# Performance work log

Hardware: AMD Instinct MI355X
Metric: run time of the kernel (lower is better)

Reference implementation:

```python
import jax, jax.numpy as jnp
import numpy as np

NEG_SLOPE = 0.2
# relation r: src node type SRC[r], dst node type DST[r]; 0=Drug, 1=Disease
# order: TREATS, TREATED_BY, HAS_CONTRAIND, CONTRAIND_BY, HAS_PARENTCODE, HAS_CHILDCODE, INTERACTS
SRC = (0, 1, 0, 1, 1, 1, 0)
DST = (1, 0, 1, 0, 1, 1, 0)

N_DRUG, N_DIS, D_IN, HID, OUT, E = 20000, 40000, 256, 128, 128, 150000


def _gat(x_src, x_dst, edge_index, Ws, Wd, a_s, a_d, b):
    # single-head PyG GATConv, add_self_loops=False
    hs = x_src @ Ws                      # [Ns, H]
    hd = x_dst @ Wd                      # [Nd, H]
    src, dst = edge_index[0], edge_index[1]
    n_dst = x_dst.shape[0]
    alpha_src = hs @ a_s                 # [Ns]
    alpha_dst = hd @ a_d                 # [Nd]
    alpha = jax.nn.leaky_relu(alpha_src[src] + alpha_dst[dst], NEG_SLOPE)  # [E]
    amax = jax.ops.segment_max(alpha, dst, num_segments=n_dst)
    amax = jnp.where(jnp.isfinite(amax), amax, 0.0)
    ex = jnp.exp(alpha - amax[dst])
    denom = jax.ops.segment_sum(ex, dst, num_segments=n_dst)
    coef = ex / (denom[dst] + 1e-16)     # per-destination softmax (PyG softmax)
    out = jax.ops.segment_sum(hs[src] * coef[:, None], dst, num_segments=n_dst)
    return out + b


def _hetero_layer(xd, xi, edges, Ws, Wd, a_s, a_d, b):
    feats = (xd, xi)
    H = b.shape[1]
    outs = [jnp.zeros((xd.shape[0], H), xd.dtype), jnp.zeros((xi.shape[0], H), xi.dtype)]
    for r in range(7):
        o = _gat(feats[SRC[r]], feats[DST[r]], edges[r], Ws[r], Wd[r], a_s[r], a_d[r], b[r])
        outs[DST[r]] = outs[DST[r]] + o   # HeteroConv aggr='sum'
    return outs[0], outs[1]


def setup_inputs() -> dict:
    key = jax.random.key(0)
    ks = jax.random.split(key, 32)
    x_drug = jax.random.normal(ks[0], (N_DRUG, D_IN), jnp.float32)
    x_disease = jax.random.normal(ks[1], (N_DIS, D_IN), jnp.float32)
    nsz = (N_DRUG, N_DIS)
    edges = []
    for r in range(7):
        s = jax.random.randint(ks[2 + 2 * r], (E,), 0, nsz[SRC[r]], jnp.int32)
        d = jax.random.randint(ks[3 + 2 * r], (E,), 0, nsz[DST[r]], jnp.int32)
        edges.append(jnp.stack([s, d]))
    s = 0.1
    W1s = s * jax.random.normal(ks[16], (7, D_IN, HID), jnp.float32)
    W1d = s * jax.random.normal(ks[17], (7, D_IN, HID), jnp.float32)
    W1d = W1d.at[6].set(W1s[6])  # INTERACTS shares src/dst lin (GATConv(-1,...))
    a1s = s * jax.random.normal(ks[18], (7, HID), jnp.float32)
    a1d = s * jax.random.normal(ks[19], (7, HID), jnp.float32)
    b1 = jnp.zeros((7, HID), jnp.float32)
    W2s = s * jax.random.normal(ks[20], (7, HID, HID), jnp.float32)
    W2d = s * jax.random.normal(ks[21], (7, HID, HID), jnp.float32)
    W2d = W2d.at[6].set(W2s[6])
    a2s = s * jax.random.normal(ks[22], (7, HID), jnp.float32)
    a2d = s * jax.random.normal(ks[23], (7, HID), jnp.float32)
    b2 = jnp.zeros((7, HID), jnp.float32)
    W_drug = s * jax.random.normal(ks[24], (HID, OUT), jnp.float32)
    b_drug = jnp.zeros((OUT,), jnp.float32)
    W_dis = s * jax.random.normal(ks[25], (HID, OUT), jnp.float32)
    b_dis = jnp.zeros((OUT,), jnp.float32)
    return {"x_drug": x_drug, "x_disease": x_disease,
            "e_treats": edges[0], "e_treated_by": edges[1], "e_contraind": edges[2],
            "e_contraind_by": edges[3], "e_parent": edges[4], "e_child": edges[5],
            "e_interacts": edges[6],
            "W1s": W1s, "W1d": W1d, "a1s": a1s, "a1d": a1d, "b1": b1,
            "W2s": W2s, "W2d": W2d, "a2s": a2s, "a2d": a2d, "b2": b2,
            "W_drug": W_drug, "b_drug": b_drug, "W_dis": W_dis, "b_dis": b_dis}


def reference(x_drug, x_disease, e_treats, e_treated_by, e_contraind, e_contraind_by,
              e_parent, e_child, e_interacts,
              W1s, W1d, a1s, a1d, b1, W2s, W2d, a2s, a2d, b2,
              W_drug, b_drug, W_dis, b_dis):
    edges = (e_treats, e_treated_by, e_contraind, e_contraind_by, e_parent, e_child, e_interacts)
    xd, xi = _hetero_layer(x_drug, x_disease, edges, W1s, W1d, a1s, a1d, b1)
    xd, xi = jax.nn.relu(xd), jax.nn.relu(xi)  # dropout is identity (eval mode)
    xd, xi = _hetero_layer(xd, xi, edges, W2s, W2d, a2s, a2d, b2)
    out_drug = jax.nn.relu(xd @ W_drug + b_drug)
    out_disease = jax.nn.relu(xi @ W_dis + b_dis)
    return out_drug, out_disease
```

## Files before the change

kernel.cpp:

```cpp
#include <hip/hip_runtime.h>
#include <stdint.h>

#define NDRUG 20000
#define NDIS  40000
#define HID   128
#define NE    150000
#define NREL  7
#define RPSTR (NDIS + 1)
#define NS_TOT (NREL * RPSTR)

typedef unsigned short ushort_t;
typedef __attribute__((ext_vector_type(8))) short bf16x8;
typedef __attribute__((ext_vector_type(4))) float f32x4;
typedef const __attribute__((address_space(1))) void gv_t;
typedef __attribute__((address_space(3))) void lv_t;

__device__ __forceinline__ ushort_t f2bf(float f) {
  unsigned u = __float_as_uint(f);
  u += 0x7FFFu + ((u >> 16) & 1u);
  return (ushort_t)(u >> 16);
}
__device__ __forceinline__ float bf2f(ushort_t h) {
  return __uint_as_float(((unsigned)h) << 16);
}

struct GemmJob { const ushort_t* A; const ushort_t* BT; const float* bias; void* C; int M, N; };

template<bool BIAS, bool RELU, bool BF16OUT>
__global__ __launch_bounds__(256) void gemm_dual(GemmJob j0, GemmJob j1, int gx0, int K)
{
  __shared__ ushort_t As[128 * 32];
  __shared__ ushort_t Bs[128 * 32];
  const bool first = blockIdx.x < (unsigned)gx0;
  const GemmJob J = first ? j0 : j1;
  const int bx = first ? blockIdx.x : blockIdx.x - gx0;
  if ((int)blockIdx.y * 128 >= J.N) return;
  const int tid = threadIdx.x;
  const int m0 = bx * 128;
  const int n0 = blockIdx.y * 128;
  const int wave = tid >> 6, lane = tid & 63;
  const int wm = wave & 1, wn = wave >> 1;
  const int l15 = lane & 15, lk = lane >> 4;

  const int rowS = wave * 16 + (lane >> 2);
  const int chunk = (lane & 3) * 8;
  const int grA0 = min(m0 + rowS, J.M - 1);
  const int grA1 = min(m0 + rowS + 64, J.M - 1);
  const ushort_t* ga0 = J.A + (size_t)grA0 * K + chunk;
  const ushort_t* ga1 = J.A + (size_t)grA1 * K + chunk;
  const ushort_t* gb0 = J.BT + (size_t)(n0 + rowS) * K + chunk;
  const ushort_t* gb1 = J.BT + (size_t)(n0 + rowS + 64) * K + chunk;

  f32x4 acc[4][4] = {};

  for (int k0 = 0; k0 < K; k0 += 32) {
    __syncthreads();
    __builtin_amdgcn_global_load_lds((gv_t*)(ga0 + k0), (lv_t*)(As + wave * 512), 16, 0, 0);
    __builtin_amdgcn_global_load_lds((gv_t*)(ga1 + k0), (lv_t*)(As + wave * 512 + 2048), 16, 0, 0);
    __builtin_amdgcn_global_load_lds((gv_t*)(gb0 + k0), (lv_t*)(Bs + wave * 512), 16, 0, 0);
    __builtin_amdgcn_global_load_lds((gv_t*)(gb1 + k0), (lv_t*)(Bs + wave * 512 + 2048), 16, 0, 0);
    __syncthreads();

    bf16x8 af[4], bfg[4];
    #pragma unroll
    for (int m = 0; m < 4; ++m)
      af[m] = *reinterpret_cast<const bf16x8*>(&As[(wm * 64 + m * 16 + l15) * 32 + lk * 8]);
    #pragma unroll
    for (int n = 0; n < 4; ++n)
      bfg[n] = *reinterpret_cast<const bf16x8*>(&Bs[(wn * 64 + n * 16 + l15) * 32 + lk * 8]);
    #pragma unroll
    for (int m = 0; m < 4; ++m)
      #pragma unroll
      for (int n = 0; n < 4; ++n)
        acc[m][n] = __builtin_amdgcn_mfma_f32_16x16x32_bf16(af[m], bfg[n], acc[m][n], 0, 0, 0);
  }

  #pragma unroll
  for (int m = 0; m < 4; ++m) {
    int rbase = m0 + wm * 64 + m * 16 + lk * 4;
    #pragma unroll
    for (int n = 0; n < 4; ++n) {
      int col = n0 + wn * 64 + n * 16 + l15;
      float bv = 0.f;
      if (BIAS) bv = J.bias[col];
      #pragma unroll
      for (int j = 0; j < 4; ++j) {
        int row = rbase + j;
        if (row >= J.M) continue;
        float v = acc[m][n][j] + bv;
        if (RELU) v = fmaxf(v, 0.f);
        if (BF16OUT) ((ushort_t*)J.C)[(size_t)row * J.N + col] = f2bf(v);
        else         ((float*)J.C)[(size_t)row * J.N + col] = v;
      }
    }
  }
}

__global__ void build_wcat2(const float* __restrict__ WA, ushort_t* __restrict__ outA,
                            int ncolA, int4 relsA,
                            const float* __restrict__ WB, ushort_t* __restrict__ outB,
                            int ncolB, int4 relsB, int K)
{
  int id = blockIdx.x * 256 + threadIdx.x;
  const float* W; ushort_t* out; int ncol; int4 rels;
  int totA = K * ncolA;
  if (id < totA) { W = WA; out = outA; ncol = ncolA; rels = relsA; }
  else {
    id -= totA;
    if (id >= K * ncolB) return;
    W = WB; out = outB; ncol = ncolB; rels = relsB;
  }
  int k = id / ncol, c = id - k * ncol;
  int rr = (&rels.x)[c >> 7];
  out[(size_t)c * K + k] = f2bf(W[((size_t)rr * K + k) * HID + (c & 127)]);
}

__global__ __launch_bounds__(256) void wvec_kernel(
    const float* __restrict__ Wsrc, const float* __restrict__ as_,
    const float* __restrict__ Wdst, const float* __restrict__ ad_,
    float* __restrict__ wv, int K)
{
  int slot = blockIdx.x;
  int r = slot % NREL;
  const float* W = (slot < NREL ? Wsrc : Wdst) + (size_t)r * K * HID;
  const float* a = (slot < NREL ? as_ : ad_) + r * HID;
  int wave = threadIdx.x >> 6, lane = threadIdx.x & 63;
  int k = blockIdx.y * 4 + wave;
  if (k >= K) return;
  float s = W[(size_t)k * HID + lane] * a[lane]
          + W[(size_t)k * HID + 64 + lane] * a[64 + lane];
  #pragma unroll
  for (int off = 32; off; off >>= 1) s += __shfl_xor(s, off);
  if (lane == 0) wv[slot * 256 + k] = s;
}

__global__ void cvt2_f32_bf16(const float* __restrict__ inA, ushort_t* __restrict__ outA, int n8A,
                              const float* __restrict__ inB, ushort_t* __restrict__ outB, int n8B)
{
  int i = blockIdx.x * 256 + threadIdx.x;
  const float* in; ushort_t* out;
  if (i < n8A) { in = inA; out = outA; }
  else {
    i -= n8A;
    if (i >= n8B) return;
    in = inB; out = outB;
  }
  float4 a = reinterpret_cast<const float4*>(in)[2 * i];
  float4 b = reinterpret_cast<const float4*>(in)[2 * i + 1];
  ushort_t r[8] = {f2bf(a.x), f2bf(a.y), f2bf(a.z), f2bf(a.w),
                   f2bf(b.x), f2bf(b.y), f2bf(b.z), f2bf(b.w)};
  reinterpret_cast<uint4*>(out)[i] = *reinterpret_cast<uint4*>(r);
}

struct AlphaJobs { int wslot[8]; int outOff[8]; };

template<int K>
__global__ __launch_bounds__(256) void alpha_dual(
    const ushort_t* __restrict__ XD, const ushort_t* __restrict__ XI,
    const float* __restrict__ wv, float* __restrict__ outBase,
    AlphaJobs jd, AlphaJobs ji, int gbD)
{
  const bool isD = blockIdx.x < (unsigned)gbD;
  const ushort_t* X = isD ? XD : XI;
  const int N = isD ? NDRUG : NDIS;
  const AlphaJobs jobs = isD ? jd : ji;
  int i = (isD ? blockIdx.x : blockIdx.x - gbD) * 256 + threadIdx.x;
  if (i >= N) return;
  float acc[8];
  #pragma unroll
  for (int v = 0; v < 8; ++v) acc[v] = 0.f;
  const ushort_t* xp = X + (size_t)i * K;
  for (int k = 0; k < K; k += 8) {
    uint4 u = *reinterpret_cast<const uint4*>(xp + k);
    unsigned uu[4] = {u.x, u.y, u.z, u.w};
    float xf[8];
    #pragma unroll
    for (int q = 0; q < 4; ++q) {
      xf[2 * q]     = __uint_as_float(uu[q] << 16);
      xf[2 * q + 1] = __uint_as_float(uu[q] & 0xFFFF0000u);
    }
    #pragma unroll
    for (int v = 0; v < 8; ++v) {
      const float* wp = wv + jobs.wslot[v] * 256 + k;
      #pragma unroll
      for (int q = 0; q < 8; ++q) acc[v] += xf[q] * wp[q];
    }
  }
  #pragma unroll
  for (int v = 0; v < 8; ++v) outBase[jobs.outOff[v] + i] = acc[v];
}

struct RelIdx { const int* src[NREL]; const int* dst[NREL]; };
struct NdArr  { int nd[NREL]; };

__global__ void zero_ints(int* __restrict__ p, int n) {
  int i = blockIdx.x * 256 + threadIdx.x;
  if (i < n) p[i] = 0;
}
__global__ void hist_k(RelIdx ri, int* __restrict__ counts) {
  int e = blockIdx.x * 256 + threadIdx.x;
  int r = blockIdx.y;
  if (e >= NE) return;
  atomicAdd(&counts[r * RPSTR + ri.dst[r][e]], 1);
}
__global__ __launch_bounds__(256) void scan_blk(const int* __restrict__ in,
                                                int* __restrict__ partial,
                                                int* __restrict__ bsum, int n)
{
  __shared__ int ts[256];
  int t = threadIdx.x;
  int base = blockIdx.x * 1024 + t * 4;
  int v[4];
  #pragma unroll
  for (int i = 0; i < 4; ++i) v[i] = (base + i < n) ? in[base + i] : 0;
  int s = v[0] + v[1] + v[2] + v[3];
  ts[t] = s; __syncthreads();
  for (int off = 1; off < 256; off <<= 1) {
    int x = (t >= off) ? ts[t - off] : 0;
    __syncthreads();
    ts[t] += x;
    __syncthreads();
  }
  int run = ts[t] - s;
  #pragma unroll
  for (int i = 0; i < 4; ++i) {
    if (base + i < n) partial[base + i] = run;
    run += v[i];
  }
  if (t == 255) bsum[blockIdx.x] = ts[255];
}
__global__ __launch_bounds__(512) void scan_top(int* __restrict__ bsum, int nb) {
  __shared__ int ts[512];
  int t = threadIdx.x;
  int v = (t < nb) ? bsum[t] : 0;
  ts[t] = v; __syncthreads();
  for (int off = 1; off < 512; off <<= 1) {
    int x = (t >= off) ? ts[t - off] : 0;
    __syncthreads();
    ts[t] += x;
    __syncthreads();
  }
  if (t < nb) bsum[t] = ts[t] - v;
}
__global__ void scan_add(const int* __restrict__ partial, const int* __restrict__ bsum,
                         int* __restrict__ rowptr, int* __restrict__ cursor, int n)
{
  int i = blockIdx.x * 256 + threadIdx.x;
  if (i >= n) return;
  int v = partial[i] + bsum[i >> 10];
  rowptr[i] = v; cursor[i] = v;
}
__global__ void fill_k(RelIdx ri, int* __restrict__ cursor, int* __restrict__ colsrc) {
  int e = blockIdx.x * 256 + threadIdx.x;
  int r = blockIdx.y;
  if (e >= NE) return;
  int d = ri.dst[r][e];
  int pos = atomicAdd(&cursor[r * RPSTR + d], 1);
  colsrc[pos] = ri.src[r][e];
}

__global__ __launch_bounds__(256) void coef_k(
    const int* __restrict__ rowptr, const int* __restrict__ colsrc,
    float2* __restrict__ pack, const float* __restrict__ alphaB,
    float* __restrict__ invden, NdArr nds)
{
  int d = blockIdx.x * 256 + threadIdx.x;
  int r = blockIdx.y;
  if (d >= nds.nd[r]) return;
  int beg = rowptr[r * RPSTR + d], end = rowptr[r * RPSTR + d + 1];
  if (beg == end) return;
  const float ad = alphaB[(NREL + r) * NDIS + d];
  const float* as = alphaB + (size_t)r * NDIS;
  int deg = end - beg;
  float sum = 0.f;
  if (deg <= 16) {
    float av[16]; int sv[16];
    float m = -1e30f;
    #pragma unroll
    for (int i = 0; i < 16; ++i) {
      float a = -1e30f; int s = 0;
      if (i < deg) {
        s = colsrc[beg + i];
        a = as[s] + ad;
        a = a > 0.f ? a : 0.2f * a;
      }
      av[i] = a; sv[i] = s;
      m = fmaxf(m, a);
    }
    #pragma unroll
    for (int i = 0; i < 16; ++i) {
      if (i < deg) {
        float ex = __expf(av[i] - m);
        float2 pk; pk.x = ex; pk.y = __int_as_float(sv[i]);
        pack[beg + i] = pk;
        sum += ex;
      }
    }
  } else {
    float m = -1e30f;
    for (int i = beg; i < end; ++i) {
      float a = as[colsrc[i]] + ad;
      a = a > 0.f ? a : 0.2f * a;
      m = fmaxf(m, a);
    }
    for (int i = beg; i < end; ++i) {
      int s = colsrc[i];
      float a = as[s] + ad;
      a = a > 0.f ? a : 0.2f * a;
      float ex = __expf(a - m);
      float2 pk; pk.x = ex; pk.y = __int_as_float(s);
      pack[i] = pk;
      sum += ex;
    }
  }
  invden[r * NDIS + d] = 1.f / (sum + 1e-16f);
}

struct PvRel { int rel; int rowptr_off; const ushort_t* hs; int hst; int hoff; };
struct PvParams { PvRel dr[3]; PvRel di[4]; };

template<bool RELU>
__global__ __launch_bounds__(256) void pv_multi(
    PvParams P, const int* __restrict__ rowptr, const float2* __restrict__ pack,
    const float* __restrict__ invden, const float* __restrict__ bias,
    ushort_t* __restrict__ outD, ushort_t* __restrict__ outI, int nbD)
{
  const int wave = threadIdx.x >> 6, lane = threadIdx.x & 63;
  const int grp = lane >> 4, l15 = lane & 15;
  const int c0 = l15 * 8;
  const bool isD = blockIdx.x < (unsigned)nbD;
  const int d = (isD ? blockIdx.x : blockIdx.x - nbD) * 4 + wave;
  const int Nd = isD ? NDRUG : NDIS;
  if (d >= Nd) return;
  const int nr = isD ? 3 : 4;
  float acc[8] = {};

  #pragma unroll
  for (int q = 0; q < 4; ++q) {
    if (q >= nr) break;
    const PvRel R = isD ? P.dr[q] : P.di[q];
    const int beg = rowptr[R.rowptr_off + d];
    const int end = rowptr[R.rowptr_off + d + 1];
    if (beg == end) continue;
    const ushort_t* hsb = R.hs + R.hoff + c0;
    const int hst = R.hst;
    float p[8] = {};
    for (int c = beg; c < end; c += 8) {
      const int e0 = c + grp, e1 = c + 4 + grp;
      const float2 k0 = pack[min(e0, end - 1)];
      const float2 k1 = pack[min(e1, end - 1)];
      const float cf0 = (e0 < end) ? k0.x : 0.f;
      const float cf1 = (e1 < end) ? k1.x : 0.f;
      const uint4 h0 = *reinterpret_cast<const uint4*>(
          hsb + (size_t)__float_as_int(k0.y) * hst);
      const uint4 h1 = *reinterpret_cast<const uint4*>(
          hsb + (size_t)__float_as_int(k1.y) * hst);
      const unsigned w0[4] = {h0.x, h0.y, h0.z, h0.w};
      const unsigned w1[4] = {h1.x, h1.y, h1.z, h1.w};
      #pragma unroll
      for (int t = 0; t < 4; ++t) {
        p[2 * t]     += cf0 * __uint_as_float(w0[t] << 16);
        p[2 * t + 1] += cf0 * __uint_as_float(w0[t] & 0xFFFF0000u);
        p[2 * t]     += cf1 * __uint_as_float(w1[t] << 16);
        p[2 * t + 1] += cf1 * __uint_as_float(w1[t] & 0xFFFF0000u);
      }
    }
    const float inv = invden[R.rel * NDIS + d];
    #pragma unroll
    for (int t = 0; t < 8; ++t) acc[t] += p[t] * inv;
  }

  #pragma unroll
  for (int t = 0; t < 8; ++t) {
    acc[t] += __shfl_xor(acc[t], 16);
    acc[t] += __shfl_xor(acc[t], 32);
  }

  if (grp == 0) {
    #pragma unroll
    for (int q = 0; q < 4; ++q) {
      if (q >= nr) break;
      const PvRel R = isD ? P.dr[q] : P.di[q];
      const float4 b0 = *reinterpret_cast<const float4*>(&bias[R.rel * HID + c0]);
      const float4 b1 = *reinterpret_cast<const float4*>(&bias[R.rel * HID + c0 + 4]);
      acc[0] += b0.x; acc[1] += b0.y; acc[2] += b0.z; acc[3] += b0.w;
      acc[4] += b1.x; acc[5] += b1.y; acc[6] += b1.z; acc[7] += b1.w;
    }
    if (RELU) {
      #pragma unroll
      for (int t = 0; t < 8; ++t) acc[t] = fmaxf(acc[t], 0.f);
    }
    ushort_t o[8];
    #pragma unroll
    for (int t = 0; t < 8; ++t) o[t] = f2bf(acc[t]);
    ushort_t* out = isD ? outD : outI;
    *reinterpret_cast<uint4*>(out + (size_t)d * HID + c0) = *reinterpret_cast<uint4*>(o);
  }
}

static const int DSTh[NREL] = {1, 0, 1, 0, 1, 1, 0};

struct WsPlan {
  ushort_t *xdb1, *xib1, *xd1b, *xi1b, *xd2b, *xi2b;
  ushort_t *hs_d, *hs_i, *wcatT_d, *wcatT_i, *wfinT_d, *wfinT_i;
  float2* pack;
  float *alphaB, *wv, *invden;
  int *counts, *rowptr, *cursor, *colsrc, *bsum;
  size_t total_bytes;
};

static WsPlan plan_ws(void* d_ws) {
  WsPlan p;
  ushort_t* s = (ushort_t*)d_ws;
  p.xdb1 = s;     s += (size_t)NDRUG * 256;
  p.xib1 = s;     s += (size_t)NDIS * 256;
  p.xd1b = s;     s += (size_t)NDRUG * HID;
  p.xi1b = s;     s += (size_t)NDIS * HID;
  p.hs_d = s;     s += (size_t)NDRUG * 384;
  p.hs_i = s;     s += (size_t)NDIS * 512;
  p.wcatT_d = s;  s += 384 * 256;
  p.wcatT_i = s;  s += 512 * 256;
  p.wfinT_d = s;  s += 128 * 128;
  p.wfinT_i = s;  s += 128 * 128;
  p.xd2b = p.xdb1;
  p.xi2b = p.xib1;
  p.pack = (float2*)s;
  float2* e = p.pack + (size_t)NREL * NE;
  float* f = (float*)e;
  p.alphaB = f;   f += (size_t)15 * NDIS;
  p.wv = f;       f += 14 * 256;
  p.invden = f;   f += (size_t)NREL * NDIS;
  int* q = (int*)f;
  p.counts = q;   q += NS_TOT;
  p.rowptr = q;   q += NS_TOT;
  p.cursor = q;   q += NS_TOT;
  p.colsrc = q;   q += NREL * NE;
  p.bsum = q;     q += 512;
  p.total_bytes = (size_t)((char*)q - (char*)d_ws);
  return p;
}

static void run_layer(const ushort_t* XDb, const ushort_t* XIb, int K,
                      const float* Wsrc, const float* Wdst,
                      const float* as_, const float* ad_, const float* bias,
                      ushort_t* outDb, ushort_t* outIb, bool relu,
                      const WsPlan& p, hipStream_t stream)
{
  int4 rd = make_int4(0, 2, 6, 0);
  int4 ri4 = make_int4(1, 3, 4, 5);
  build_wcat2<<<(K * 896 + 255) / 256, 256, 0, stream>>>(
      Wsrc, p.wcatT_d, 384, rd, Wsrc, p.wcatT_i, 512, ri4, K);
  wvec_kernel<<<dim3(14, K / 4), 256, 0, stream>>>(Wsrc, as_, Wdst, ad_, p.wv, K);

  AlphaJobs jd = {};
  jd.wslot[0] = 0;     jd.outOff[0] = 0 * NDIS;
  jd.wslot[1] = 2;     jd.outOff[1] = 2 * NDIS;
  jd.wslot[2] = 6;     jd.outOff[2] = 6 * NDIS;
  jd.wslot[3] = 7 + 1; jd.outOff[3] = (7 + 1) * NDIS;
  jd.wslot[4] = 7 + 3; jd.outOff[4] = (7 + 3) * NDIS;
  jd.wslot[5] = 7 + 6; jd.outOff[5] = (7 + 6) * NDIS;
  jd.wslot[6] = 0;     jd.outOff[6] = 14 * NDIS;
  jd.wslot[7] = 0;     jd.outOff[7] = 14 * NDIS;
  AlphaJobs ji = {};
  ji.wslot[0] = 1;     ji.outOff[0] = 1 * NDIS;
  ji.wslot[1] = 3;     ji.outOff[1] = 3 * NDIS;
  ji.wslot[2] = 4;     ji.outOff[2] = 4 * NDIS;
  ji.wslot[3] = 5;     ji.outOff[3] = 5 * NDIS;
  ji.wslot[4] = 7 + 0; ji.outOff[4] = (7 + 0) * NDIS;
  ji.wslot[5] = 7 + 2; ji.outOff[5] = (7 + 2) * NDIS;
  ji.wslot[6] = 7 + 4; ji.outOff[6] = (7 + 4) * NDIS;
  ji.wslot[7] = 7 + 5; ji.outOff[7] = (7 + 5) * NDIS;
  int gbD = (NDRUG + 255) / 256, gbI = (NDIS + 255) / 256;
  if (K == 256)
    alpha_dual<256><<<gbD + gbI, 256, 0, stream>>>(XDb, XIb, p.wv, p.alphaB, jd, ji, gbD);
  else
    alpha_dual<128><<<gbD + gbI, 256, 0, stream>>>(XDb, XIb, p.wv, p.alphaB, jd, ji, gbD);

  GemmJob g0 = {XDb, p.wcatT_d, nullptr, p.hs_d, NDRUG, 384};
  GemmJob g1 = {XIb, p.wcatT_i, nullptr, p.hs_i, NDIS, 512};
  int gx0 = (NDRUG + 127) / 128, gx1 = (NDIS + 127) / 128;
  gemm_dual<false, false, true><<<dim3(gx0 + gx1, 4), 256, 0, stream>>>(g0, g1, gx0, K);

  NdArr nds;
  for (int r = 0; r < NREL; ++r) nds.nd[r] = DSTh[r] == 0 ? NDRUG : NDIS;
  coef_k<<<dim3((NDIS + 255) / 256, NREL), 256, 0, stream>>>(
      p.rowptr, p.colsrc, p.pack, p.alphaB, p.invden, nds);

  PvParams P;
  P.dr[0] = {1, 1 * RPSTR, p.hs_i, 512, 0};
  P.dr[1] = {3, 3 * RPSTR, p.hs_i, 512, 128};
  P.dr[2] = {6, 6 * RPSTR, p.hs_d, 384, 256};
  P.di[0] = {0, 0 * RPSTR, p.hs_d, 384, 0};
  P.di[1] = {2, 2 * RPSTR, p.hs_d, 384, 128};
  P.di[2] = {4, 4 * RPSTR, p.hs_i, 512, 256};
  P.di[3] = {5, 5 * RPSTR, p.hs_i, 512, 384};
  int nbD = (NDRUG + 3) / 4, nbI = (NDIS + 3) / 4;
  if (relu)
    pv_multi<true><<<nbD + nbI, 256, 0, stream>>>(
        P, p.rowptr, p.pack, p.invden, bias, outDb, outIb, nbD);
  else
    pv_multi<false><<<nbD + nbI, 256, 0, stream>>>(
        P, p.rowptr, p.pack, p.invden, bias, outDb, outIb, nbD);
}

extern "C" void kernel_launch(void* const* d_in, const int* in_sizes, int n_in,
                              void* d_out, int out_size, void* d_ws, size_t ws_size,
                              hipStream_t stream) {
  const float* x_drug = (const float*)d_in[0];
  const float* x_dis  = (const float*)d_in[1];
  RelIdx ri;
  for (int r = 0; r < NREL; ++r) {
    const int* e = (const int*)d_in[2 + r];
    ri.src[r] = e; ri.dst[r] = e + NE;
  }
  const float* W1s = (const float*)d_in[9];
  const float* W1d = (const float*)d_in[10];
  const float* a1s = (const float*)d_in[11];
  const float* a1d = (const float*)d_in[12];
  const float* b1  = (const float*)d_in[13];
  const float* W2s = (const float*)d_in[14];
  const float* W2d = (const float*)d_in[15];
  const float* a2s = (const float*)d_in[16];
  const float* a2d = (const float*)d_in[17];
  const float* b2  = (const float*)d_in[18];
  const float* Wdr = (const float*)d_in[19];
  const float* bdr = (const float*)d_in[20];
  const float* Wdi = (const float*)d_in[21];
  const float* bdi = (const float*)d_in[22];

  WsPlan p = plan_ws(d_ws);
  if (p.total_bytes > ws_size) return;

  cvt2_f32_bf16<<<((NDRUG + NDIS) * 256 / 8 + 255) / 256, 256, 0, stream>>>(
      x_drug, p.xdb1, NDRUG * 256 / 8, x_dis, p.xib1, NDIS * 256 / 8);

  zero_ints<<<(NS_TOT + 255) / 256, 256, 0, stream>>>(p.counts, NS_TOT);
  dim3 ge((NE + 255) / 256, NREL);
  hist_k<<<ge, 256, 0, stream>>>(ri, p.counts);
  int nb = (NS_TOT + 1023) / 1024;
  scan_blk<<<nb, 256, 0, stream>>>(p.counts, p.cursor, p.bsum, NS_TOT);
  scan_top<<<1, 512, 0, stream>>>(p.bsum, nb);
  scan_add<<<(NS_TOT + 255) / 256, 256, 0, stream>>>(p.cursor, p.bsum, p.rowptr, p.cursor, NS_TOT);
  fill_k<<<ge, 256, 0, stream>>>(ri, p.cursor, p.colsrc);

  run_layer(p.xdb1, p.xib1, 256, W1s, W1d, a1s, a1d, b1, p.xd1b, p.xi1b, true, p, stream);
  run_layer(p.xd1b, p.xi1b, 128, W2s, W2d, a2s, a2d, b2, p.xd2b, p.xi2b, false, p, stream);

  int4 r0 = make_int4(0, 0, 0, 0);
  build_wcat2<<<(128 * 128 * 2 + 255) / 256, 256, 0, stream>>>(
      Wdr, p.wfinT_d, 128, r0, Wdi, p.wfinT_i, 128, r0, 128);
  float* out = (float*)d_out;
  GemmJob f0 = {p.xd2b, p.wfinT_d, bdr, out, NDRUG, 128};
  GemmJob f1 = {p.xi2b, p.wfinT_i, bdi, out + (size_t)NDRUG * HID, NDIS, 128};
  int gx0 = (NDRUG + 127) / 128, gx1 = (NDIS + 127) / 128;
  gemm_dual<true, true, false><<<dim3(gx0 + gx1, 1), 256, 0, stream>>>(f0, f1, gx0, 128);
}
```

Before: 480.2 us.

## Widen GEMM N-tile, fold softmax normalization into coef, merge scan stages, restructure aggregation

The GEMM now computes 128x256 tiles per block, halving grid.y and reusing each A tile across twice as many columns, at the cost of more accumulator registers. The coefficient kernel writes pre-normalized softmax weights, so the separate invden buffer and its per-relation read in aggregation go away. The scan_top and scan_add kernels are merged into one scan_fin kernel that reduces preceding block sums itself. pv_multi is restructured to one wave per destination, with each lane owning two columns and iterating edges four at a time, which removes the cross-lane shuffle reduction but issues narrower 4-byte gathers.

```diff
diff --git a/kernel.cpp b/kernel.cpp
--- a/kernel.cpp
+++ b/kernel.cpp
@@ -30,48 +30,49 @@
 __global__ __launch_bounds__(256) void gemm_dual(GemmJob j0, GemmJob j1, int gx0, int K)
 {
   __shared__ ushort_t As[128 * 32];
-  __shared__ ushort_t Bs[128 * 32];
+  __shared__ ushort_t Bs[256 * 32];
   const bool first = blockIdx.x < (unsigned)gx0;
   const GemmJob J = first ? j0 : j1;
   const int bx = first ? blockIdx.x : blockIdx.x - gx0;
-  if ((int)blockIdx.y * 128 >= J.N) return;
+  const int m0 = bx * 128;
+  const int n0 = blockIdx.y * 256;
+  if (n0 >= J.N) return;
   const int tid = threadIdx.x;
-  const int m0 = bx * 128;
-  const int n0 = blockIdx.y * 128;
   const int wave = tid >> 6, lane = tid & 63;
   const int wm = wave & 1, wn = wave >> 1;
   const int l15 = lane & 15, lk = lane >> 4;
 
   const int rowS = wave * 16 + (lane >> 2);
   const int chunk = (lane & 3) * 8;
-  const int grA0 = min(m0 + rowS, J.M - 1);
-  const int grA1 = min(m0 + rowS + 64, J.M - 1);
-  const ushort_t* ga0 = J.A + (size_t)grA0 * K + chunk;
-  const ushort_t* ga1 = J.A + (size_t)grA1 * K + chunk;
-  const ushort_t* gb0 = J.BT + (size_t)(n0 + rowS) * K + chunk;
-  const ushort_t* gb1 = J.BT + (size_t)(n0 + rowS + 64) * K + chunk;
-
-  f32x4 acc[4][4] = {};
+  const ushort_t* ga0 = J.A + (size_t)min(m0 + rowS, J.M - 1) * K + chunk;
+  const ushort_t* ga1 = J.A + (size_t)min(m0 + rowS + 64, J.M - 1) * K + chunk;
+  const ushort_t* gb[4];
+  #pragma unroll
+  for (int i = 0; i < 4; ++i)
+    gb[i] = J.BT + (size_t)min(n0 + rowS + i * 64, J.N - 1) * K + chunk;
+
+  f32x4 acc[4][8] = {};
 
   for (int k0 = 0; k0 < K; k0 += 32) {
     __syncthreads();
     __builtin_amdgcn_global_load_lds((gv_t*)(ga0 + k0), (lv_t*)(As + wave * 512), 16, 0, 0);
     __builtin_amdgcn_global_load_lds((gv_t*)(ga1 + k0), (lv_t*)(As + wave * 512 + 2048), 16, 0, 0);
-    __builtin_amdgcn_global_load_lds((gv_t*)(gb0 + k0), (lv_t*)(Bs + wave * 512), 16, 0, 0);
-    __builtin_amdgcn_global_load_lds((gv_t*)(gb1 + k0), (lv_t*)(Bs + wave * 512 + 2048), 16, 0, 0);
+    #pragma unroll
+    for (int i = 0; i < 4; ++i)
+      __builtin_amdgcn_global_load_lds((gv_t*)(gb[i] + k0), (lv_t*)(Bs + wave * 512 + i * 2048), 16, 0, 0);
     __syncthreads();
 
-    bf16x8 af[4], bfg[4];
+    bf16x8 af[4], bfg[8];
     #pragma unroll
     for (int m = 0; m < 4; ++m)
       af[m] = *reinterpret_cast<const bf16x8*>(&As[(wm * 64 + m * 16 + l15) * 32 + lk * 8]);
     #pragma unroll
-    for (int n = 0; n < 4; ++n)
-      bfg[n] = *reinterpret_cast<const bf16x8*>(&Bs[(wn * 64 + n * 16 + l15) * 32 + lk * 8]);
+    for (int n = 0; n < 8; ++n)
+      bfg[n] = *reinterpret_cast<const bf16x8*>(&Bs[(wn * 128 + n * 16 + l15) * 32 + lk * 8]);
     #pragma unroll
     for (int m = 0; m < 4; ++m)
       #pragma unroll
-      for (int n = 0; n < 4; ++n)
+      for (int n = 0; n < 8; ++n)
         acc[m][n] = __builtin_amdgcn_mfma_f32_16x16x32_bf16(af[m], bfg[n], acc[m][n], 0, 0, 0);
   }
 
@@ -79,8 +80,9 @@
   for (int m = 0; m < 4; ++m) {
     int rbase = m0 + wm * 64 + m * 16 + lk * 4;
     #pragma unroll
-    for (int n = 0; n < 4; ++n) {
-      int col = n0 + wn * 64 + n * 16 + l15;
+    for (int n = 0; n < 8; ++n) {
+      int col = n0 + wn * 128 + n * 16 + l15;
+      if (col >= J.N) continue;
       float bv = 0.f;
       if (BIAS) bv = J.bias[col];
       #pragma unroll
@@ -229,26 +231,29 @@
   }
   if (t == 255) bsum[blockIdx.x] = ts[255];
 }
-__global__ __launch_bounds__(512) void scan_top(int* __restrict__ bsum, int nb) {
+__global__ __launch_bounds__(512) void scan_fin(const int* __restrict__ partial,
+                                                const int* __restrict__ bsum,
+                                                int* __restrict__ rowptr,
+                                                int* __restrict__ cursor, int n)
+{
   __shared__ int ts[512];
   int t = threadIdx.x;
-  int v = (t < nb) ? bsum[t] : 0;
-  ts[t] = v; __syncthreads();
-  for (int off = 1; off < 512; off <<= 1) {
-    int x = (t >= off) ? ts[t - off] : 0;
+  ts[t] = (t < (int)blockIdx.x) ? bsum[t] : 0;
+  __syncthreads();
+  #pragma unroll
+  for (int off = 256; off; off >>= 1) {
+    if (t < off) ts[t] += ts[t + off];
     __syncthreads();
-    ts[t] += x;
-    __syncthreads();
-  }
-  if (t < nb) bsum[t] = ts[t] - v;
-}
-__global__ void scan_add(const int* __restrict__ partial, const int* __restrict__ bsum,
-                         int* __restrict__ rowptr, int* __restrict__ cursor, int n)
-{
-  int i = blockIdx.x * 256 + threadIdx.x;
-  if (i >= n) return;
-  int v = partial[i] + bsum[i >> 10];
-  rowptr[i] = v; cursor[i] = v;
+  }
+  int base = ts[0];
+  #pragma unroll
+  for (int i = 0; i < 2; ++i) {
+    int idx = blockIdx.x * 1024 + t + i * 512;
+    if (idx < n) {
+      int v = partial[idx] + base;
+      rowptr[idx] = v; cursor[idx] = v;
+    }
+  }
 }
 __global__ void fill_k(RelIdx ri, int* __restrict__ cursor, int* __restrict__ colsrc) {
   int e = blockIdx.x * 256 + threadIdx.x;
@@ -261,8 +266,7 @@
 
 __global__ __launch_bounds__(256) void coef_k(
     const int* __restrict__ rowptr, const int* __restrict__ colsrc,
-    float2* __restrict__ pack, const float* __restrict__ alphaB,
-    float* __restrict__ invden, NdArr nds)
+    float2* __restrict__ pack, const float* __restrict__ alphaB, NdArr nds)
 {
   int d = blockIdx.x * 256 + threadIdx.x;
   int r = blockIdx.y;
@@ -272,7 +276,6 @@
   const float ad = alphaB[(NREL + r) * NDIS + d];
   const float* as = alphaB + (size_t)r * NDIS;
   int deg = end - beg;
-  float sum = 0.f;
   if (deg <= 16) {
     float av[16]; int sv[16];
     float m = -1e30f;
@@ -287,13 +290,21 @@
       av[i] = a; sv[i] = s;
       m = fmaxf(m, a);
     }
+    float sum = 0.f;
     #pragma unroll
     for (int i = 0; i < 16; ++i) {
       if (i < deg) {
         float ex = __expf(av[i] - m);
-        float2 pk; pk.x = ex; pk.y = __int_as_float(sv[i]);
+        av[i] = ex;
+        sum += ex;
+      }
+    }
+    float inv = 1.f / (sum + 1e-16f);
+    #pragma unroll
+    for (int i = 0; i < 16; ++i) {
+      if (i < deg) {
+        float2 pk; pk.x = av[i] * inv; pk.y = __int_as_float(sv[i]);
         pack[beg + i] = pk;
-        sum += ex;
       }
     }
   } else {
@@ -303,6 +314,7 @@
       a = a > 0.f ? a : 0.2f * a;
       m = fmaxf(m, a);
     }
+    float sum = 0.f;
     for (int i = beg; i < end; ++i) {
       int s = colsrc[i];
       float a = as[s] + ad;
@@ -312,8 +324,9 @@
       pack[i] = pk;
       sum += ex;
     }
-  }
-  invden[r * NDIS + d] = 1.f / (sum + 1e-16f);
+    float inv = 1.f / (sum + 1e-16f);
+    for (int i = beg; i < end; ++i) ((float*)pack)[2 * (size_t)i] *= inv;
+  }
 }
 
 struct PvRel { int rel; int rowptr_off; const ushort_t* hs; int hst; int hoff; };
@@ -322,18 +335,17 @@
 template<bool RELU>
 __global__ __launch_bounds__(256) void pv_multi(
     PvParams P, const int* __restrict__ rowptr, const float2* __restrict__ pack,
-    const float* __restrict__ invden, const float* __restrict__ bias,
+    const float* __restrict__ bias,
     ushort_t* __restrict__ outD, ushort_t* __restrict__ outI, int nbD)
 {
   const int wave = threadIdx.x >> 6, lane = threadIdx.x & 63;
-  const int grp = lane >> 4, l15 = lane & 15;
-  const int c0 = l15 * 8;
+  const int c0 = 2 * lane;
   const bool isD = blockIdx.x < (unsigned)nbD;
   const int d = (isD ? blockIdx.x : blockIdx.x - nbD) * 4 + wave;
   const int Nd = isD ? NDRUG : NDIS;
   if (d >= Nd) return;
   const int nr = isD ? 3 : 4;
-  float acc[8] = {};
+  float acc0 = 0.f, acc1 = 0.f;
 
   #pragma unroll
   for (int q = 0; q < 4; ++q) {
@@ -344,58 +356,40 @@
     if (beg == end) continue;
     const ushort_t* hsb = R.hs + R.hoff + c0;
     const int hst = R.hst;
-    float p[8] = {};
-    for (int c = beg; c < end; c += 8) {
-      const int e0 = c + grp, e1 = c + 4 + grp;
-      const float2 k0 = pack[min(e0, end - 1)];
-      const float2 k1 = pack[min(e1, end - 1)];
-      const float cf0 = (e0 < end) ? k0.x : 0.f;
-      const float cf1 = (e1 < end) ? k1.x : 0.f;
-      const uint4 h0 = *reinterpret_cast<const uint4*>(
-          hsb + (size_t)__float_as_int(k0.y) * hst);
-      const uint4 h1 = *reinterpret_cast<const uint4*>(
-          hsb + (size_t)__float_as_int(k1.y) * hst);
-      const unsigned w0[4] = {h0.x, h0.y, h0.z, h0.w};
-      const unsigned w1[4] = {h1.x, h1.y, h1.z, h1.w};
+    for (int c = beg; c < end; c += 4) {
+      float cf[4]; int si[4];
       #pragma unroll
-      for (int t = 0; t < 4; ++t) {
-        p[2 * t]     += cf0 * __uint_as_float(w0[t] << 16);
-        p[2 * t + 1] += cf0 * __uint_as_float(w0[t] & 0xFFFF0000u);
-        p[2 * t]     += cf1 * __uint_as_float(w1[t] << 16);
-        p[2 * t + 1] += cf1 * __uint_as_float(w1[t] & 0xFFFF0000u);
+      for (int j = 0; j < 4; ++j) {
+        int idx = (c + j < end) ? c + j : end - 1;
+        float2 pk = pack[idx];
+        cf[j] = (c + j < end) ? pk.x : 0.f;
+        si[j] = __float_as_int(pk.y);
       }
-    }
-    const float inv = invden[R.rel * NDIS + d];
-    #pragma unroll
-    for (int t = 0; t < 8; ++t) acc[t] += p[t] * inv;
-  }
-
-  #pragma unroll
-  for (int t = 0; t < 8; ++t) {
-    acc[t] += __shfl_xor(acc[t], 16);
-    acc[t] += __shfl_xor(acc[t], 32);
-  }
-
-  if (grp == 0) {
-    #pragma unroll
-    for (int q = 0; q < 4; ++q) {
-      if (q >= nr) break;
-      const PvRel R = isD ? P.dr[q] : P.di[q];
-      const float4 b0 = *reinterpret_cast<const float4*>(&bias[R.rel * HID + c0]);
-      const float4 b1 = *reinterpret_cast<const float4*>(&bias[R.rel * HID + c0 + 4]);
-      acc[0] += b0.x; acc[1] += b0.y; acc[2] += b0.z; acc[3] += b0.w;
-      acc[4] += b1.x; acc[5] += b1.y; acc[6] += b1.z; acc[7] += b1.w;
-    }
-    if (RELU) {
+      ushort2 hv[4];
       #pragma unroll
-      for (int t = 0; t < 8; ++t) acc[t] = fmaxf(acc[t], 0.f);
-    }
-    ushort_t o[8];
-    #pragma unroll
-    for (int t = 0; t < 8; ++t) o[t] = f2bf(acc[t]);
-    ushort_t* out = isD ? outD : outI;
-    *reinterpret_cast<uint4*>(out + (size_t)d * HID + c0) = *reinterpret_cast<uint4*>(o);
-  }
+      for (int j = 0; j < 4; ++j)
+        hv[j] = *reinterpret_cast<const ushort2*>(hsb + (size_t)si[j] * hst);
+      #pragma unroll
+      for (int j = 0; j < 4; ++j) {
+        acc0 += cf[j] * bf2f(hv[j].x);
+        acc1 += cf[j] * bf2f(hv[j].y);
+      }
+    }
+  }
+
+  float b0 = 0.f, b1 = 0.f;
+  #pragma unroll
+  for (int q = 0; q < 4; ++q) {
+    if (q >= nr) break;
+    const PvRel R = isD ? P.dr[q] : P.di[q];
+    const float2 bv = *reinterpret_cast<const float2*>(&bias[R.rel * HID + c0]);
+    b0 += bv.x; b1 += bv.y;
+  }
+  acc0 += b0; acc1 += b1;
+  if (RELU) { acc0 = fmaxf(acc0, 0.f); acc1 = fmaxf(acc1, 0.f); }
+  ushort2 o; o.x = f2bf(acc0); o.y = f2bf(acc1);
+  ushort_t* out = isD ? outD : outI;
+  *reinterpret_cast<ushort2*>(out + (size_t)d * HID + c0) = o;
 }
 
 static const int DSTh[NREL] = {1, 0, 1, 0, 1, 1, 0};
@@ -404,7 +398,7 @@
   ushort_t *xdb1, *xib1, *xd1b, *xi1b, *xd2b, *xi2b;
   ushort_t *hs_d, *hs_i, *wcatT_d, *wcatT_i, *wfinT_d, *wfinT_i;
   float2* pack;
-  float *alphaB, *wv, *invden;
+  float *alphaB, *wv;
   int *counts, *rowptr, *cursor, *colsrc, *bsum;
   size_t total_bytes;
 };
@@ -429,7 +423,6 @@
   float* f = (float*)e;
   p.alphaB = f;   f += (size_t)15 * NDIS;
   p.wv = f;       f += 14 * 256;
-  p.invden = f;   f += (size_t)NREL * NDIS;
   int* q = (int*)f;
   p.counts = q;   q += NS_TOT;
   p.rowptr = q;   q += NS_TOT;
@@ -479,12 +472,12 @@
   GemmJob g0 = {XDb, p.wcatT_d, nullptr, p.hs_d, NDRUG, 384};
   GemmJob g1 = {XIb, p.wcatT_i, nullptr, p.hs_i, NDIS, 512};
   int gx0 = (NDRUG + 127) / 128, gx1 = (NDIS + 127) / 128;
-  gemm_dual<false, false, true><<<dim3(gx0 + gx1, 4), 256, 0, stream>>>(g0, g1, gx0, K);
+  gemm_dual<false, false, true><<<dim3(gx0 + gx1, 2), 256, 0, stream>>>(g0, g1, gx0, K);
 
   NdArr nds;
   for (int r = 0; r < NREL; ++r) nds.nd[r] = DSTh[r] == 0 ? NDRUG : NDIS;
   coef_k<<<dim3((NDIS + 255) / 256, NREL), 256, 0, stream>>>(
-      p.rowptr, p.colsrc, p.pack, p.alphaB, p.invden, nds);
+      p.rowptr, p.colsrc, p.pack, p.alphaB, nds);
 
   PvParams P;
   P.dr[0] = {1, 1 * RPSTR, p.hs_i, 512, 0};
@@ -497,10 +490,10 @@
   int nbD = (NDRUG + 3) / 4, nbI = (NDIS + 3) / 4;
   if (relu)
     pv_multi<true><<<nbD + nbI, 256, 0, stream>>>(
-        P, p.rowptr, p.pack, p.invden, bias, outDb, outIb, nbD);
+        P, p.rowptr, p.pack, bias, outDb, outIb, nbD);
   else
     pv_multi<false><<<nbD + nbI, 256, 0, stream>>>(
-        P, p.rowptr, p.pack, p.invden, bias, outDb, outIb, nbD);
+        P, p.rowptr, p.pack, bias, outDb, outIb, nbD);
 }
 
 extern "C" void kernel_launch(void* const* d_in, const int* in_sizes, int n_in,
@@ -539,8 +532,7 @@
   hist_k<<<ge, 256, 0, stream>>>(ri, p.counts);
   int nb = (NS_TOT + 1023) / 1024;
   scan_blk<<<nb, 256, 0, stream>>>(p.counts, p.cursor, p.bsum, NS_TOT);
-  scan_top<<<1, 512, 0, stream>>>(p.bsum, nb);
-  scan_add<<<(NS_TOT + 255) / 256, 256, 0, stream>>>(p.cursor, p.bsum, p.rowptr, p.cursor, NS_TOT);
+  scan_fin<<<nb, 512, 0, stream>>>(p.cursor, p.bsum, p.rowptr, p.cursor, NS_TOT);
   fill_k<<<ge, 256, 0, stream>>>(ri, p.cursor, p.colsrc);
 
   run_layer(p.xdb1, p.xib1, 256, W1s, W1d, a1s, a1d, b1, p.xd1b, p.xi1b, true, p, stream);
```

Result: slower. 561.1 us (+16.8%).
